# Kernel optimization log

Measured on AMD Instinct MI355X. Metric: run time of the kernel, lower is better.

## Reference

```python
import jax, jax.numpy as jnp
import numpy as np

N = 50000   # nodes
E = 800000  # edges
IN, H, OUT = 64, 512, 128


def _lin_init(key, out_dim, in_dim):
    kw, kb = jax.random.split(key)
    bound = 1.0 / np.sqrt(in_dim)
    W = jax.random.uniform(kw, (out_dim, in_dim), jnp.float32, -bound, bound)
    b = jax.random.uniform(kb, (out_dim,), jnp.float32, -bound, bound)
    return W, b


def setup_inputs() -> dict:
    key = jax.random.key(0)
    ks = jax.random.split(key, 10)
    x = jax.random.normal(ks[0], (N, IN), jnp.float32)
    edge_index = jax.random.randint(ks[1], (2, E), 0, N, jnp.int64)
    W_s1, b_s1 = _lin_init(ks[2], H, IN)
    W_s2, b_s2 = _lin_init(ks[3], H, H)
    W_s3, b_s3 = _lin_init(ks[4], H, H)
    W_s4, b_s4 = _lin_init(ks[5], H, H)
    W_m1, b_m1 = _lin_init(ks[6], OUT, H)
    W_m2, b_m2 = _lin_init(ks[7], OUT, OUT)
    W_l1, b_l1 = _lin_init(ks[8], OUT, H)
    W_l2, b_l2 = _lin_init(ks[9], OUT, OUT)
    return {"x": x, "edge_index": edge_index,
            "W_s1": W_s1, "b_s1": b_s1, "W_s2": W_s2, "b_s2": b_s2,
            "W_s3": W_s3, "b_s3": b_s3, "W_s4": W_s4, "b_s4": b_s4,
            "W_m1": W_m1, "b_m1": b_m1, "W_m2": W_m2, "b_m2": b_m2,
            "W_l1": W_l1, "b_l1": b_l1, "W_l2": W_l2, "b_l2": b_l2}


def _aggregate(h, src, dst):
    # GINConv with default eps=0: (1+eps)*x + sum_{j in N(i)} x_j
    return h + jax.ops.segment_sum(h[src], dst, num_segments=N)


def reference(x, edge_index,
              W_s1, b_s1, W_s2, b_s2, W_s3, b_s3, W_s4, b_s4,
              W_m1, b_m1, W_m2, b_m2, W_l1, b_l1, W_l2, b_l2):
    src, dst = edge_index[0], edge_index[1]
    lrelu = lambda v: jax.nn.leaky_relu(v, 0.1)

    def mlp_shared(h):
        h = lrelu(h @ W_s1.T + b_s1)
        h = lrelu(h @ W_s2.T + b_s2)
        h = lrelu(h @ W_s3.T + b_s3)
        return h @ W_s4.T + b_s4

    def mlp_mu(h):
        return jax.nn.relu(h @ W_m1.T + b_m1) @ W_m2.T + b_m2

    def mlp_logvar(h):
        return jax.nn.relu(h @ W_l1.T + b_l1) @ W_l2.T + b_l2

    h = jax.nn.relu(mlp_shared(_aggregate(x, src, dst)))
    mu = mlp_mu(_aggregate(h, src, dst))
    logvar = mlp_logvar(_aggregate(h, src, dst))
    return (mu, logvar)
```

## Files before the change

### kernel.cpp

```cpp
#include <hip/hip_runtime.h>
#include <hip/hip_bf16.h>
#include <stdint.h>

#define N_NODES 50000
#define N_PAD   50048
#define E_EDGES 800000
#define MT      391

typedef __bf16 bf16x8 __attribute__((ext_vector_type(8)));
typedef __bf16 bf16x4 __attribute__((ext_vector_type(4)));
typedef float  f32x4  __attribute__((ext_vector_type(4)));

__global__ void count_deg(const int* __restrict__ ei, int* __restrict__ cnt) {
    int e = blockIdx.x * blockDim.x + threadIdx.x;
    if (e < E_EDGES) atomicAdd(&cnt[ei[E_EDGES + e]], 1);
}

#define SCAN_B 1024
__global__ void scan_block(const int* __restrict__ cnt, int* __restrict__ ptr,
                           int* __restrict__ bsum, int n) {
    __shared__ int buf[SCAN_B];
    int i = blockIdx.x * SCAN_B + threadIdx.x;
    int v = (i < n) ? cnt[i] : 0;
    buf[threadIdx.x] = v;
    __syncthreads();
    #pragma unroll
    for (int off = 1; off < SCAN_B; off <<= 1) {
        int t = (threadIdx.x >= (unsigned)off) ? buf[threadIdx.x - off] : 0;
        __syncthreads();
        buf[threadIdx.x] += t;
        __syncthreads();
    }
    if (i < n) ptr[i] = buf[threadIdx.x] - v;
    if (threadIdx.x == SCAN_B - 1) bsum[blockIdx.x] = buf[SCAN_B - 1];
}

__global__ void scan_bsums(int* __restrict__ bsum, int* __restrict__ boff, int nb,
                           int* __restrict__ total_out) {
    __shared__ int buf[64];
    int v = ((int)threadIdx.x < nb) ? bsum[threadIdx.x] : 0;
    buf[threadIdx.x] = v;
    __syncthreads();
    #pragma unroll
    for (int off = 1; off < 64; off <<= 1) {
        int t = (threadIdx.x >= (unsigned)off) ? buf[threadIdx.x - off] : 0;
        __syncthreads();
        buf[threadIdx.x] += t;
        __syncthreads();
    }
    if ((int)threadIdx.x < nb) boff[threadIdx.x] = buf[threadIdx.x] - v;
    if (threadIdx.x == 63) *total_out = buf[63];
}

__global__ void scan_add(int* __restrict__ ptr, const int* __restrict__ boff, int n) {
    int i = blockIdx.x * SCAN_B + threadIdx.x;
    if (i < n) ptr[i] += boff[blockIdx.x];
}

__global__ void fill_csr(const int* __restrict__ ei, const int* __restrict__ ptr,
                         int* __restrict__ cursor, int* __restrict__ col) {
    int e = blockIdx.x * blockDim.x + threadIdx.x;
    if (e < E_EDGES) {
        int dst = ei[E_EDGES + e];
        int pos = ptr[dst] + atomicAdd(&cursor[dst], 1);
        col[pos] = ei[e];
    }
}

#define XN      3200000
#define WTOT    983040
__global__ void cvt_all(const float* __restrict__ x,
                        const float* __restrict__ Ws1, const float* __restrict__ Ws2,
                        const float* __restrict__ Ws3, const float* __restrict__ Ws4,
                        const float* __restrict__ Wm1, const float* __restrict__ Wl1,
                        const float* __restrict__ Wm2, const float* __restrict__ Wl2,
                        __bf16* __restrict__ xb, __bf16* __restrict__ wbuf) {
    int i = blockIdx.x * blockDim.x + threadIdx.x;
    if (i < XN) { xb[i] = (__bf16)x[i]; return; }
    int j = i - XN;
    if (j >= WTOT) return;
    const float* s; int o;
    if      (j <  32768) { s = Ws1; o = j; }
    else if (j < 294912) { s = Ws2; o = j -  32768; }
    else if (j < 557056) { s = Ws3; o = j - 294912; }
    else if (j < 819200) { s = Ws4; o = j - 557056; }
    else if (j < 884736) { s = Wm1; o = j - 819200; }
    else if (j < 950272) { s = Wl1; o = j - 884736; }
    else if (j < 966656) { s = Wm2; o = j - 950272; }
    else                 { s = Wl2; o = j - 966656; }
    wbuf[j] = (__bf16)s[o];
}

__global__ void agg0_gather(const __bf16* __restrict__ xb, const int* __restrict__ ptr,
                            const int* __restrict__ col, __bf16* __restrict__ out) {
    int node = blockIdx.x * 4 + (threadIdx.x >> 6);
    int lane = threadIdx.x & 63;
    if (node >= N_PAD) return;
    long o = (long)node * 64 + lane;
    if (node >= N_NODES) { out[o] = (__bf16)0.0f; return; }
    float acc = (float)xb[o];
    int e0 = ptr[node], e1 = ptr[node + 1];
    int e = e0;
    for (; e + 8 <= e1; e += 8) {
        int c[8];
        #pragma unroll
        for (int u = 0; u < 8; ++u) c[u] = col[e + u];
        float v[8];
        #pragma unroll
        for (int u = 0; u < 8; ++u) v[u] = (float)xb[(long)c[u] * 64 + lane];
        #pragma unroll
        for (int u = 0; u < 8; ++u) acc += v[u];
    }
    for (; e < e1; ++e) acc += (float)xb[(long)col[e] * 64 + lane];
    out[o] = (__bf16)acc;
}

__global__ void aggt_gather(const __bf16* __restrict__ t, const int* __restrict__ ptr,
                            const int* __restrict__ col, const float* __restrict__ b_m1,
                            const float* __restrict__ b_l1, __bf16* __restrict__ p) {
    int node = blockIdx.x * 4 + (threadIdx.x >> 6);
    int lane = threadIdx.x & 63;
    if (node >= N_NODES) return;
    const int f0 = lane * 4;
    bf16x4 s = *(const bf16x4*)&t[(long)node * 256 + f0];
    float a0 = (float)s[0], a1 = (float)s[1], a2 = (float)s[2], a3 = (float)s[3];
    int e0 = ptr[node], e1 = ptr[node + 1];
    int e = e0;
    for (; e + 8 <= e1; e += 8) {
        int c[8];
        #pragma unroll
        for (int u = 0; u < 8; ++u) c[u] = col[e + u];
        bf16x4 v[8];
        #pragma unroll
        for (int u = 0; u < 8; ++u) v[u] = *(const bf16x4*)&t[(long)c[u] * 256 + f0];
        #pragma unroll
        for (int u = 0; u < 8; ++u) {
            a0 += (float)v[u][0]; a1 += (float)v[u][1];
            a2 += (float)v[u][2]; a3 += (float)v[u][3];
        }
    }
    for (; e < e1; ++e) {
        bf16x4 v = *(const bf16x4*)&t[(long)col[e] * 256 + f0];
        a0 += (float)v[0]; a1 += (float)v[1]; a2 += (float)v[2]; a3 += (float)v[3];
    }
    float b0, b1, b2, b3;
    if (f0 < 128) { b0 = b_m1[f0]; b1 = b_m1[f0+1]; b2 = b_m1[f0+2]; b3 = b_m1[f0+3]; }
    else          { b0 = b_l1[f0-128]; b1 = b_l1[f0-127]; b2 = b_l1[f0-126]; b3 = b_l1[f0-125]; }
    bf16x4 r;
    r[0] = (__bf16)fmaxf(a0 + b0, 0.0f);
    r[1] = (__bf16)fmaxf(a1 + b1, 0.0f);
    r[2] = (__bf16)fmaxf(a2 + b2, 0.0f);
    r[3] = (__bf16)fmaxf(a3 + b3, 0.0f);
    *(bf16x4*)&p[(long)node * 256 + f0] = r;
}

__device__ __forceinline__ void gl_lds16(const __bf16* g, __bf16* l) {
    __builtin_amdgcn_global_load_lds(
        (const __attribute__((address_space(1))) uint32_t*)g,
        (__attribute__((address_space(3))) uint32_t*)l, 16, 0, 0);
}

template <int NCOL>
__device__ __forceinline__ void swizzle_xy(int bid, int& x, int& y) {
    int grp  = bid / (8 * NCOL);
    int rem  = bid - grp * (8 * NCOL);
    int base = grp * 8;
    int width = MT - base; if (width > 8) width = 8;
    x = base + rem % width;
    y = rem / width;
}

template <int ACT, bool BIAS, bool OUT_BF16, bool MCHK>
__device__ __forceinline__ void gemm_core(
    const __bf16* __restrict__ A, int lda, const __bf16* __restrict__ W,
    const float* __restrict__ bias, void* __restrict__ Cout, int ldc,
    int K, long Mstore, long blockRow, int blockCol,
    __bf16* __restrict__ smem) {
    __bf16* As = smem;
    __bf16* Ws = smem + 8192;
    const int tid  = threadIdx.x;
    const int wid  = tid >> 6;
    const int lane = tid & 63;
    const int wm = (wid >> 1) << 6;
    const int wn = (wid & 1) << 6;

    f32x4 acc[4][4];
    #pragma unroll
    for (int i = 0; i < 4; ++i)
        #pragma unroll
        for (int j = 0; j < 4; ++j) acc[i][j] = (f32x4)0.0f;

    const int srow = lane >> 3;
    const int skg  = (lane & 7) ^ srow;
    const __bf16* gA[4]; const __bf16* gW[4];
    __bf16 *lA[4], *lW[4];
    #pragma unroll
    for (int i = 0; i < 4; ++i) {
        int c = wid * 4 + i;
        gA[i] = A + (blockRow + c * 8 + srow) * (long)lda + skg * 8;
        gW[i] = W + ((long)blockCol + c * 8 + srow) * (long)K + skg * 8;
        lA[i] = As + c * 512;
        lW[i] = Ws + c * 512;
    }

    const int rA = lane & 15;
    const int q  = lane >> 4;
    const int r7 = rA & 7;

    for (int k0 = 0; k0 < K; k0 += 64) {
        #pragma unroll
        for (int i = 0; i < 4; ++i) gl_lds16(gA[i] + k0, lA[i]);
        #pragma unroll
        for (int i = 0; i < 4; ++i) gl_lds16(gW[i] + k0, lW[i]);
        __syncthreads();

        #pragma unroll
        for (int s = 0; s < 2; ++s) {
            const int slot = ((s * 4 + q) ^ r7) * 8;
            bf16x8 af[4], bf[4];
            #pragma unroll
            for (int mi = 0; mi < 4; ++mi)
                af[mi] = *(const bf16x8*)&As[(wm + mi * 16 + rA) * 64 + slot];
            #pragma unroll
            for (int ni = 0; ni < 4; ++ni)
                bf[ni] = *(const bf16x8*)&Ws[(wn + ni * 16 + rA) * 64 + slot];
            #pragma unroll
            for (int mi = 0; mi < 4; ++mi)
                #pragma unroll
                for (int ni = 0; ni < 4; ++ni)
                    acc[mi][ni] = __builtin_amdgcn_mfma_f32_16x16x32_bf16(
                        af[mi], bf[ni], acc[mi][ni], 0, 0, 0);
        }
        __syncthreads();
    }

    const int ccol = lane & 15;
    const int crow = (lane >> 4) << 2;
    if (OUT_BF16 && !MCHK) {
        #pragma unroll
        for (int mi = 0; mi < 4; ++mi) {
            #pragma unroll
            for (int ni = 0; ni < 4; ++ni) {
                int gc = wn + ni * 16 + ccol;
                float bv = BIAS ? bias[blockCol + gc] : 0.0f;
                #pragma unroll
                for (int r = 0; r < 4; ++r) {
                    float v = acc[mi][ni][r] + bv;
                    if (ACT == 1) v = (v > 0.0f) ? v : 0.1f * v;
                    else if (ACT == 2) v = fmaxf(v, 0.0f);
                    smem[(wm + mi * 16 + crow + r) * 128 + gc] = (__bf16)v;
                }
            }
        }
        __syncthreads();
        #pragma unroll
        for (int i = 0; i < 8; ++i) {
            int o   = (i * 256 + tid) * 8;
            int row = o >> 7;
            int co  = o & 127;
            *(bf16x8*)((__bf16*)Cout + (blockRow + row) * (long)ldc + blockCol + co) =
                *(const bf16x8*)&smem[o];
        }
    } else {
        #pragma unroll
        for (int mi = 0; mi < 4; ++mi) {
            #pragma unroll
            for (int ni = 0; ni < 4; ++ni) {
                long gr0 = blockRow + wm + mi * 16 + crow;
                int  gc  = blockCol + wn + ni * 16 + ccol;
                float bv = BIAS ? bias[gc] : 0.0f;
                #pragma unroll
                for (int r = 0; r < 4; ++r) {
                    long gr = gr0 + r;
                    if (!MCHK || gr < Mstore) {
                        float v = acc[mi][ni][r] + bv;
                        if (ACT == 1) v = (v > 0.0f) ? v : 0.1f * v;
                        else if (ACT == 2) v = fmaxf(v, 0.0f);
                        if (OUT_BF16) ((__bf16*)Cout)[gr * ldc + gc] = (__bf16)v;
                        else          ((float*)Cout)[gr * ldc + gc] = v;
                    }
                }
            }
        }
    }
}

template <int NCOL, int ACT, bool BIAS, bool OUT_BF16, bool MCHK>
__global__ __launch_bounds__(256) void gemm_bt(
    const __bf16* __restrict__ A, int lda, const __bf16* __restrict__ W,
    const float* __restrict__ bias, void* __restrict__ Cout, int ldc,
    int K, long Mstore) {
    __shared__ __bf16 smem[128 * 128];
    int x, y;
    swizzle_xy<NCOL>(blockIdx.x, x, y);
    gemm_core<ACT, BIAS, OUT_BF16, MCHK>(A, lda, W, bias, Cout, ldc, K, Mstore,
                                         (long)x * 128, y * 128, smem);
}

__global__ __launch_bounds__(256) void gemm_heads(
    const __bf16* __restrict__ p, const __bf16* __restrict__ wm2,
    const float* __restrict__ b_m2, float* __restrict__ mu,
    const __bf16* __restrict__ wl2, const float* __restrict__ b_l2,
    float* __restrict__ lv) {
    __shared__ __bf16 smem[128 * 128];
    int x, hd;
    swizzle_xy<2>(blockIdx.x, x, hd);
    if (hd == 0)
        gemm_core<0, true, false, true>(p, 256, wm2, b_m2, mu, 128, 128, N_NODES,
                                        (long)x * 128, 0, smem);
    else
        gemm_core<0, true, false, true>(p + 128, 256, wl2, b_l2, lv, 128, 128, N_NODES,
                                        (long)x * 128, 0, smem);
}

extern "C" void kernel_launch(void* const* d_in, const int* in_sizes, int n_in,
                              void* d_out, int out_size, void* d_ws, size_t ws_size,
                              hipStream_t stream) {
    const float* x    = (const float*)d_in[0];
    const int*   ei   = (const int*)d_in[1];
    const float* W_s1 = (const float*)d_in[2];
    const float* b_s1 = (const float*)d_in[3];
    const float* W_s2 = (const float*)d_in[4];
    const float* b_s2 = (const float*)d_in[5];
    const float* W_s3 = (const float*)d_in[6];
    const float* b_s3 = (const float*)d_in[7];
    const float* W_s4 = (const float*)d_in[8];
    const float* b_s4 = (const float*)d_in[9];
    const float* W_m1 = (const float*)d_in[10];
    const float* b_m1 = (const float*)d_in[11];
    const float* W_m2 = (const float*)d_in[12];
    const float* b_m2 = (const float*)d_in[13];
    const float* W_l1 = (const float*)d_in[14];
    const float* b_l1 = (const float*)d_in[15];
    const float* W_l2 = (const float*)d_in[16];
    const float* b_l2 = (const float*)d_in[17];

    char* ws = (char*)d_ws;
    size_t off = 0;
    auto carve = [&](size_t bytes) -> void* {
        void* p = ws + off;
        off = (off + bytes + 255) & ~(size_t)255;
        return p;
    };
    int* cnt  = (int*)carve((size_t)N_NODES * 4);
    int* cur  = (int*)carve((size_t)N_NODES * 4);
    int* ptr  = (int*)carve((size_t)(N_NODES + 1) * 4);
    int* col  = (int*)carve((size_t)E_EDGES * 4);
    int* bsum = (int*)carve(64 * 4);
    int* boff = (int*)carve(64 * 4);
    __bf16* wbuf = (__bf16*)carve((size_t)WTOT * 2);
    __bf16* w1  = wbuf;
    __bf16* w2  = wbuf +  32768;
    __bf16* w3  = wbuf + 294912;
    __bf16* w4  = wbuf + 557056;
    __bf16* wml = wbuf + 819200;
    __bf16* wm2 = wbuf + 950272;
    __bf16* wl2 = wbuf + 966656;
    __bf16* xb    = (__bf16*)carve((size_t)XN * 2);
    __bf16* agg0b = (__bf16*)carve((size_t)N_PAD * 64 * 2);
    __bf16* B1    = (__bf16*)carve((size_t)N_PAD * 512 * 2);
    __bf16* B2    = (__bf16*)carve((size_t)N_PAD * 512 * 2);

    (void)hipMemsetAsync(cnt, 0, (size_t)N_NODES * 4, stream);
    (void)hipMemsetAsync(cur, 0, (size_t)N_NODES * 4, stream);

    const int NB = (N_NODES + SCAN_B - 1) / SCAN_B;
    count_deg<<<E_EDGES / 256, 256, 0, stream>>>(ei, cnt);
    scan_block<<<NB, SCAN_B, 0, stream>>>(cnt, ptr, bsum, N_NODES);
    scan_bsums<<<1, 64, 0, stream>>>(bsum, boff, NB, &ptr[N_NODES]);
    scan_add<<<NB, SCAN_B, 0, stream>>>(ptr, boff, N_NODES);
    fill_csr<<<E_EDGES / 256, 256, 0, stream>>>(ei, ptr, cur, col);

    cvt_all<<<(XN + WTOT + 255) / 256, 256, 0, stream>>>(
        x, W_s1, W_s2, W_s3, W_s4, W_m1, W_l1, W_m2, W_l2, xb, wbuf);

    agg0_gather<<<N_PAD / 4, 256, 0, stream>>>(xb, ptr, col, agg0b);

    gemm_bt<4, 1, true, true, false><<<MT * 4, 256, 0, stream>>>(agg0b, 64, w1, b_s1, B1, 512, 64, N_PAD);
    gemm_bt<4, 1, true, true, false><<<MT * 4, 256, 0, stream>>>(B1, 512, w2, b_s2, B2, 512, 512, N_PAD);
    gemm_bt<4, 1, true, true, false><<<MT * 4, 256, 0, stream>>>(B2, 512, w3, b_s3, B1, 512, 512, N_PAD);
    gemm_bt<4, 2, true, true, false><<<MT * 4, 256, 0, stream>>>(B1, 512, w4, b_s4, B2, 512, 512, N_PAD);

    __bf16* t = B1;
    gemm_bt<2, 0, false, true, false><<<MT * 2, 256, 0, stream>>>(B2, 512, wml, nullptr, t, 256, 512, N_PAD);

    __bf16* p = B2;
    aggt_gather<<<(N_NODES + 3) / 4, 256, 0, stream>>>(t, ptr, col, b_m1, b_l1, p);

    float* mu = (float*)d_out;
    float* lv = mu + (size_t)N_NODES * 128;
    gemm_heads<<<MT * 2, 256, 0, stream>>>(p, wm2, b_m2, mu, wl2, b_l2, lv);
}
```

Before: 498.0 us.

## Replace 128x128 tiled GEMMs with 64-row wide-column GEMM kernel

Adds a gemm_wide kernel in which each block owns a 64-row strip of A and loops over 256-column output tiles, with each of the four waves computing 64 columns. This replaces the 128x128-tile gemm_bt launches and their swizzled block mapping for the shared MLP and the combined mu/logvar first layer. The goal is to improve A-row reuse in cache and to give a different block count (782 blocks). In exchange, the A strip is reloaded for every column tile and the W tile reloaded per block is larger. The staged-epilogue path in gemm_core is also removed, leaving only the direct-store path for the heads kernel.

```diff
diff --git a/kernel.cpp b/kernel.cpp
--- a/kernel.cpp
+++ b/kernel.cpp
@@ -6,6 +6,7 @@
 #define N_PAD   50048
 #define E_EDGES 800000
 #define MT      391
+#define MS64    782
 
 typedef __bf16 bf16x8 __attribute__((ext_vector_type(8)));
 typedef __bf16 bf16x4 __attribute__((ext_vector_type(4)));
@@ -160,14 +161,104 @@
         (__attribute__((address_space(3))) uint32_t*)l, 16, 0, 0);
 }
 
-template <int NCOL>
-__device__ __forceinline__ void swizzle_xy(int bid, int& x, int& y) {
-    int grp  = bid / (8 * NCOL);
-    int rem  = bid - grp * (8 * NCOL);
-    int base = grp * 8;
-    int width = MT - base; if (width > 8) width = 8;
-    x = base + rem % width;
-    y = rem / width;
+template <int NCT, int ACT, bool BIAS>
+__global__ __launch_bounds__(256) void gemm_wide(
+    const __bf16* __restrict__ A, int lda, const __bf16* __restrict__ W,
+    const float* __restrict__ bias, __bf16* __restrict__ C, int ldc, int K) {
+    __shared__ __bf16 smem[20480];
+    __bf16* As = smem;
+    __bf16* Ws = smem + 4096;
+
+    const int tid  = threadIdx.x;
+    const int wid  = tid >> 6;
+    const int lane = tid & 63;
+    const long row0 = (long)blockIdx.x * 64;
+
+    const int srow = lane >> 3;
+    const int skg  = (lane & 7) ^ srow;
+    const __bf16* gA[2]; __bf16* lA[2];
+    #pragma unroll
+    for (int i = 0; i < 2; ++i) {
+        int c = wid * 2 + i;
+        gA[i] = A + (row0 + c * 8 + srow) * (long)lda + skg * 8;
+        lA[i] = As + c * 512;
+    }
+    __bf16* lW[8];
+    long gWoff[8];
+    #pragma unroll
+    for (int j = 0; j < 8; ++j) {
+        int c = wid * 8 + j;
+        lW[j] = Ws + c * 512;
+        gWoff[j] = (long)(c * 8 + srow) * K + skg * 8;
+    }
+
+    const int rA = lane & 15;
+    const int q  = lane >> 4;
+    const int r7 = rA & 7;
+    const int ccol = lane & 15;
+    const int crow = (lane >> 4) << 2;
+
+    for (int ct = 0; ct < NCT; ++ct) {
+        const __bf16* Wt = W + (long)ct * 256 * K;
+        f32x4 acc[4][4];
+        #pragma unroll
+        for (int i = 0; i < 4; ++i)
+            #pragma unroll
+            for (int j = 0; j < 4; ++j) acc[i][j] = (f32x4)0.0f;
+
+        for (int k0 = 0; k0 < K; k0 += 64) {
+            #pragma unroll
+            for (int i = 0; i < 2; ++i) gl_lds16(gA[i] + k0, lA[i]);
+            #pragma unroll
+            for (int j = 0; j < 8; ++j) gl_lds16(Wt + gWoff[j] + k0, lW[j]);
+            __syncthreads();
+
+            #pragma unroll
+            for (int s = 0; s < 2; ++s) {
+                const int slot = ((s * 4 + q) ^ r7) * 8;
+                bf16x8 af[4], bf[4];
+                #pragma unroll
+                for (int mi = 0; mi < 4; ++mi)
+                    af[mi] = *(const bf16x8*)&As[(mi * 16 + rA) * 64 + slot];
+                #pragma unroll
+                for (int ni = 0; ni < 4; ++ni)
+                    bf[ni] = *(const bf16x8*)&Ws[(wid * 64 + ni * 16 + rA) * 64 + slot];
+                #pragma unroll
+                for (int mi = 0; mi < 4; ++mi)
+                    #pragma unroll
+                    for (int ni = 0; ni < 4; ++ni)
+                        acc[mi][ni] = __builtin_amdgcn_mfma_f32_16x16x32_bf16(
+                            af[mi], bf[ni], acc[mi][ni], 0, 0, 0);
+            }
+            __syncthreads();
+        }
+
+        #pragma unroll
+        for (int mi = 0; mi < 4; ++mi) {
+            #pragma unroll
+            for (int ni = 0; ni < 4; ++ni) {
+                int gc = wid * 64 + ni * 16 + ccol;
+                float bv = BIAS ? bias[ct * 256 + gc] : 0.0f;
+                #pragma unroll
+                for (int r = 0; r < 4; ++r) {
+                    float v = acc[mi][ni][r] + bv;
+                    if (ACT == 1) v = (v > 0.0f) ? v : 0.1f * v;
+                    else if (ACT == 2) v = fmaxf(v, 0.0f);
+                    smem[(mi * 16 + crow + r) * 256 + gc] = (__bf16)v;
+                }
+            }
+        }
+        __syncthreads();
+        #pragma unroll
+        for (int i = 0; i < 8; ++i) {
+            int o   = (i * 256 + tid) * 8;
+            int row = o >> 8;
+            int co  = o & 255;
+            *(bf16x8*)(C + (row0 + row) * (long)ldc + ct * 256 + co) =
+                *(const bf16x8*)&smem[o];
+        }
+        __syncthreads();
+    }
 }
 
 template <int ACT, bool BIAS, bool OUT_BF16, bool MCHK>
@@ -236,65 +327,26 @@
 
     const int ccol = lane & 15;
     const int crow = (lane >> 4) << 2;
-    if (OUT_BF16 && !MCHK) {
-        #pragma unroll
-        for (int mi = 0; mi < 4; ++mi) {
-            #pragma unroll
-            for (int ni = 0; ni < 4; ++ni) {
-                int gc = wn + ni * 16 + ccol;
-                float bv = BIAS ? bias[blockCol + gc] : 0.0f;
-                #pragma unroll
-                for (int r = 0; r < 4; ++r) {
+    #pragma unroll
+    for (int mi = 0; mi < 4; ++mi) {
+        #pragma unroll
+        for (int ni = 0; ni < 4; ++ni) {
+            long gr0 = blockRow + wm + mi * 16 + crow;
+            int  gc  = blockCol + wn + ni * 16 + ccol;
+            float bv = BIAS ? bias[gc] : 0.0f;
+            #pragma unroll
+            for (int r = 0; r < 4; ++r) {
+                long gr = gr0 + r;
+                if (!MCHK || gr < Mstore) {
                     float v = acc[mi][ni][r] + bv;
                     if (ACT == 1) v = (v > 0.0f) ? v : 0.1f * v;
                     else if (ACT == 2) v = fmaxf(v, 0.0f);
-                    smem[(wm + mi * 16 + crow + r) * 128 + gc] = (__bf16)v;
+                    if (OUT_BF16) ((__bf16*)Cout)[gr * ldc + gc] = (__bf16)v;
+                    else          ((float*)Cout)[gr * ldc + gc] = v;
                 }
             }
         }
-        __syncthreads();
-        #pragma unroll
-        for (int i = 0; i < 8; ++i) {
-            int o   = (i * 256 + tid) * 8;
-            int row = o >> 7;
-            int co  = o & 127;
-            *(bf16x8*)((__bf16*)Cout + (blockRow + row) * (long)ldc + blockCol + co) =
-                *(const bf16x8*)&smem[o];
-        }
-    } else {
-        #pragma unroll
-        for (int mi = 0; mi < 4; ++mi) {
-            #pragma unroll
-            for (int ni = 0; ni < 4; ++ni) {
-                long gr0 = blockRow + wm + mi * 16 + crow;
-                int  gc  = blockCol + wn + ni * 16 + ccol;
-                float bv = BIAS ? bias[gc] : 0.0f;
-                #pragma unroll
-                for (int r = 0; r < 4; ++r) {
-                    long gr = gr0 + r;
-                    if (!MCHK || gr < Mstore) {
-                        float v = acc[mi][ni][r] + bv;
-                        if (ACT == 1) v = (v > 0.0f) ? v : 0.1f * v;
-                        else if (ACT == 2) v = fmaxf(v, 0.0f);
-                        if (OUT_BF16) ((__bf16*)Cout)[gr * ldc + gc] = (__bf16)v;
-                        else          ((float*)Cout)[gr * ldc + gc] = v;
-                    }
-                }
-            }
-        }
-    }
-}
-
-template <int NCOL, int ACT, bool BIAS, bool OUT_BF16, bool MCHK>
-__global__ __launch_bounds__(256) void gemm_bt(
-    const __bf16* __restrict__ A, int lda, const __bf16* __restrict__ W,
-    const float* __restrict__ bias, void* __restrict__ Cout, int ldc,
-    int K, long Mstore) {
-    __shared__ __bf16 smem[128 * 128];
-    int x, y;
-    swizzle_xy<NCOL>(blockIdx.x, x, y);
-    gemm_core<ACT, BIAS, OUT_BF16, MCHK>(A, lda, W, bias, Cout, ldc, K, Mstore,
-                                         (long)x * 128, y * 128, smem);
+    }
 }
 
 __global__ __launch_bounds__(256) void gemm_heads(
@@ -302,9 +354,9 @@
     const float* __restrict__ b_m2, float* __restrict__ mu,
     const __bf16* __restrict__ wl2, const float* __restrict__ b_l2,
     float* __restrict__ lv) {
-    __shared__ __bf16 smem[128 * 128];
-    int x, hd;
-    swizzle_xy<2>(blockIdx.x, x, hd);
+    __shared__ __bf16 smem[16384];
+    int x  = blockIdx.x >> 1;
+    int hd = blockIdx.x & 1;
     if (hd == 0)
         gemm_core<0, true, false, true>(p, 256, wm2, b_m2, mu, 128, 128, N_NODES,
                                         (long)x * 128, 0, smem);
@@ -376,13 +428,13 @@
 
     agg0_gather<<<N_PAD / 4, 256, 0, stream>>>(xb, ptr, col, agg0b);
 
-    gemm_bt<4, 1, true, true, false><<<MT * 4, 256, 0, stream>>>(agg0b, 64, w1, b_s1, B1, 512, 64, N_PAD);
-    gemm_bt<4, 1, true, true, false><<<MT * 4, 256, 0, stream>>>(B1, 512, w2, b_s2, B2, 512, 512, N_PAD);
-    gemm_bt<4, 1, true, true, false><<<MT * 4, 256, 0, stream>>>(B2, 512, w3, b_s3, B1, 512, 512, N_PAD);
-    gemm_bt<4, 2, true, true, false><<<MT * 4, 256, 0, stream>>>(B1, 512, w4, b_s4, B2, 512, 512, N_PAD);
+    gemm_wide<2, 1, true><<<MS64, 256, 0, stream>>>(agg0b, 64, w1, b_s1, B1, 512, 64);
+    gemm_wide<2, 1, true><<<MS64, 256, 0, stream>>>(B1, 512, w2, b_s2, B2, 512, 512);
+    gemm_wide<2, 1, true><<<MS64, 256, 0, stream>>>(B2, 512, w3, b_s3, B1, 512, 512);
+    gemm_wide<2, 2, true><<<MS64, 256, 0, stream>>>(B1, 512, w4, b_s4, B2, 512, 512);
 
     __bf16* t = B1;
-    gemm_bt<2, 0, false, true, false><<<MT * 2, 256, 0, stream>>>(B2, 512, wml, nullptr, t, 256, 512, N_PAD);
+    gemm_wide<1, 0, false><<<MS64, 256, 0, stream>>>(B2, 512, wml, nullptr, t, 256, 512);
 
     __bf16* p = B2;
     aggt_gather<<<(N_NODES + 3) / 4, 256, 0, stream>>>(t, ptr, col, b_m1, b_l1, p);
```

After: 527.7 us. 1.06x slower.
